# Kernel optimization log

Measured on AMD Instinct MI355X. Metric: run time of the kernel, lower is better.

## Reference

```python
import jax, jax.numpy as jnp
import numpy as np

V, E, D, B, L1, L2, C, NL = 32000, 300, 256, 64, 128, 128, 3, 10
BN_EPS = 1e-3  # tf.layers.batch_normalization default epsilon
BN_SCALE = 1.0 / np.sqrt(1.0 + BN_EPS)  # inference BN with moving mean=0, var=1


def setup_inputs() -> dict:
    key = jax.random.key(0)
    ks = iter(jax.random.split(key, 32))
    g = lambda shape, s=0.05: jax.random.normal(next(ks), shape, jnp.float32) * s
    inp = dict(
        embed_table=g((V, E), 1.0),
        W1_first=g((E, D)),            # layer 1 linear-BN-ReLU-1 (input dim = embed dim)
        W1_rest=g((NL - 1, D, D)),     # layers 2..10 linear-BN-ReLU-1
        b1=jnp.zeros((NL, D)),
        bn1_g=jnp.ones((NL, D)), bn1_b=jnp.zeros((NL, D)),
        W2=g((NL, 2 * D, D)),          # linear-BN-ReLU-2 on [x, aligned] concat
        b2=jnp.zeros((NL, D)),
        bn2_g=jnp.ones((NL, D)), bn2_b=jnp.zeros((NL, D)),
        Wg=g((NL, D, D)), bg=jnp.zeros((NL, D)),  # sigmoid gate
        Wf1=g((4 * D, 4 * D), 0.01), bf1=jnp.zeros((4 * D,)),
        Wf2=g((4 * D, 4 * D), 0.01), bf2=jnp.zeros((4 * D,)),
        Wout=g((4 * D, C)), bout=jnp.zeros((C,)),
        x1_ids=jax.random.randint(next(ks), (B, L1), 0, V, dtype=jnp.int32),
        x2_ids=jax.random.randint(next(ks), (B, L2), 0, V, dtype=jnp.int32),
    )
    return inp


def _lbr(x, W, b, g, be):
    # linear -> BN (inference: moving mean 0, var 1) -> ReLU
    y = jnp.dot(x, W) + b
    y = g * (y * BN_SCALE) + be
    return jax.nn.relu(y)


def _block(x1, x2):
    # pairwise squared euclidean distance: |a-b|^2 = |a|^2 + |b|^2 - 2 a.b
    sq1 = jnp.sum(x1 * x1, -1)                                  # [B,L1]
    sq2 = jnp.sum(x2 * x2, -1)                                  # [B,L2]
    edist = sq1[:, :, None] + sq2[:, None, :] \
        - 2.0 * jnp.einsum('bid,bjd->bij', x1, x2)              # [B,L1,L2]
    att = 1.0 / (1.0 + edist)
    # alpha = softmax(att^T) @ x1 ; beta = softmax(att) @ x2
    alpha = jnp.einsum('bji,bid->bjd',
                       jax.nn.softmax(jnp.swapaxes(att, 1, 2), axis=-1), x1)  # [B,L2,D]
    beta = jnp.einsum('bij,bjd->bid', jax.nn.softmax(att, axis=-1), x2)       # [B,L1,D]
    return alpha, beta


def reference(embed_table, W1_first, W1_rest, b1, bn1_g, bn1_b,
              W2, b2, bn2_g, bn2_b, Wg, bg,
              Wf1, bf1, Wf2, bf2, Wout, bout, x1_ids, x2_ids):
    x1 = embed_table[x1_ids]  # [B,L1,E]
    x2 = embed_table[x2_ids]  # [B,L2,E]
    for i in range(NL):
        W1 = W1_first if i == 0 else W1_rest[i - 1]
        h1 = _lbr(x1, W1, b1[i], bn1_g[i], bn1_b[i])
        h2 = _lbr(x2, W1, b1[i], bn1_g[i], bn1_b[i])
        alpha, beta = _block(h1, h2)
        v1 = _lbr(jnp.concatenate([h1, beta], -1), W2[i], b2[i], bn2_g[i], bn2_b[i])
        v2 = _lbr(jnp.concatenate([h2, alpha], -1), W2[i], b2[i], bn2_g[i], bn2_b[i])
        g1 = jax.nn.sigmoid(jnp.dot(h1, Wg[i]) + bg[i])
        g2 = jax.nn.sigmoid(jnp.dot(h2, Wg[i]) + bg[i])
        x1 = v1 * g1 + h1 * (1.0 - g1)
        x2 = v2 * g2 + h2 * (1.0 - g2)
    v = jnp.concatenate([x1.max(1), x2.max(1), x1.sum(1), x2.sum(1)], -1)  # [B,4D]
    t = jax.nn.relu(jnp.dot(v, Wf1) + bf1)   # op.linear default activation (ReLU); dropout off
    t = jax.nn.relu(jnp.dot(t, Wf2) + bf2)
    return jnp.dot(t, Wout) + bout           # logits [B,C]
```

## Files before the change

kernel.cpp:

```cpp
#include <hip/hip_runtime.h>
#include <hip/hip_bf16.h>
#include <cstddef>

#define NB 64
#define LL 128
#define EE 300
#define DD 256
#define NLAYERS 10
#define MROWS (NB * LL)

static constexpr float BN_SC = 0.9995003746877562f;

typedef unsigned short u16;
typedef __attribute__((ext_vector_type(4))) unsigned short us4;
typedef __attribute__((ext_vector_type(8))) unsigned short us8;
typedef __attribute__((ext_vector_type(8))) short bfrag;
typedef __attribute__((ext_vector_type(4))) float f4;

#define MFMA_B16(a, b, c) __builtin_amdgcn_mfma_f32_16x16x32_bf16(a, b, c, 0, 0, 0)

__device__ __forceinline__ u16 f2bf(float x) {
  union { float f; unsigned u; } v; v.f = x;
  unsigned r = v.u + 0x7FFFu + ((v.u >> 16) & 1u);
  return (u16)(r >> 16);
}
__device__ __forceinline__ float bf2f(u16 s) {
  union { unsigned u; float f; } v; v.u = (unsigned)s << 16;
  return v.f;
}
__device__ __forceinline__ float4 ld4(const float* p) { return *(const float4*)p; }

__device__ __forceinline__ void async16(void* lds, const void* g) {
  __builtin_amdgcn_global_load_lds(
      (const __attribute__((address_space(1))) unsigned int*)g,
      (__attribute__((address_space(3))) unsigned int*)lds, 16, 0, 0);
}

__device__ __forceinline__ void stage_tile(const u16* __restrict__ src, int ld,
                                           int r0, int k0, u16* lds, int t) {
  const int w = t >> 6;
  int c = w * 64 + (t & 63);
  async16((char*)lds + w * 1024,
          src + (size_t)(r0 + (c >> 2)) * ld + k0 + (c & 3) * 8);
  c += 256;
  async16((char*)lds + 4096 + w * 1024,
          src + (size_t)(r0 + (c >> 2)) * ld + k0 + (c & 3) * 8);
}

__device__ __forceinline__ void stage_tile64(const u16* __restrict__ src, int ld,
                                             int r0, int k0, u16* lds, int t) {
  const int w = t >> 6;
  const int c = t;
  async16((char*)lds + w * 1024,
          src + (size_t)(r0 + (c >> 2)) * ld + k0 + (c & 3) * 8);
}

__device__ __forceinline__ void mfma_step(const u16* As, const u16* Bs, int wm,
                                          int wn, int fr, int fq, f4 acc[4][4]) {
  bfrag a[4], b[4];
#pragma unroll
  for (int i = 0; i < 4; ++i)
    a[i] = *(const bfrag*)&As[(wm * 64 + i * 16 + fr) * 32 + fq * 8];
#pragma unroll
  for (int j = 0; j < 4; ++j)
    b[j] = *(const bfrag*)&Bs[(wn * 64 + j * 16 + fr) * 32 + fq * 8];
#pragma unroll
  for (int i = 0; i < 4; ++i)
#pragma unroll
    for (int j = 0; j < 4; ++j) acc[i][j] = MFMA_B16(a[i], b[j], acc[i][j]);
}

__device__ __forceinline__ void mfma_step_n64(const u16* As, const u16* Bs, int wm,
                                              int wn, int fr, int fq, f4 acc[4][2]) {
  bfrag a[4], b[2];
#pragma unroll
  for (int i = 0; i < 4; ++i)
    a[i] = *(const bfrag*)&As[(wm * 64 + i * 16 + fr) * 32 + fq * 8];
#pragma unroll
  for (int j = 0; j < 2; ++j)
    b[j] = *(const bfrag*)&Bs[(wn * 32 + j * 16 + fr) * 32 + fq * 8];
#pragma unroll
  for (int i = 0; i < 4; ++i)
#pragma unroll
    for (int j = 0; j < 2; ++j) acc[i][j] = MFMA_B16(a[i], b[j], acc[i][j]);
}

__device__ __forceinline__ void mfma_step2_n64(const u16* As, const u16* B2s,
                                               const u16* Bgs, int wm, int wn,
                                               int fr, int fq, f4 accv[4][2],
                                               f4 accg[4][2]) {
  bfrag a[4], b2[2], bg[2];
#pragma unroll
  for (int i = 0; i < 4; ++i)
    a[i] = *(const bfrag*)&As[(wm * 64 + i * 16 + fr) * 32 + fq * 8];
#pragma unroll
  for (int j = 0; j < 2; ++j) {
    b2[j] = *(const bfrag*)&B2s[(wn * 32 + j * 16 + fr) * 32 + fq * 8];
    bg[j] = *(const bfrag*)&Bgs[(wn * 32 + j * 16 + fr) * 32 + fq * 8];
  }
#pragma unroll
  for (int i = 0; i < 4; ++i)
#pragma unroll
    for (int j = 0; j < 2; ++j) {
      accv[i][j] = MFMA_B16(a[i], b2[j], accv[i][j]);
      accg[i][j] = MFMA_B16(a[i], bg[j], accg[i][j]);
    }
}

__device__ __forceinline__ bfrag gfrag(const u16* __restrict__ p, int ld, int row, int k) {
  return *(const bfrag*)(p + (size_t)row * ld + k);
}

__device__ __forceinline__ int eswz(int row, int colbyte) {
  return (row * 256 + colbyte) ^ ((row & 7) << 4);
}
__device__ __forceinline__ bfrag ldsE(const u16* E, int row, int colbyte) {
  return *(const bfrag*)((const char*)E + eswz(row, colbyte));
}

__device__ void txw_tile(const float* __restrict__ src, u16* __restrict__ dst,
                         int K, int N, int Kpad, int k0, int n0, int t,
                         float (*tileS)[65]) {
  __syncthreads();
  {
    const int kr = t >> 2, nc = (t & 3) * 16;
    const int k = k0 + kr;
#pragma unroll
    for (int j = 0; j < 16; j += 4) {
      float4 v = (k < K) ? ld4(src + (size_t)k * N + n0 + nc + j)
                         : make_float4(0.f, 0.f, 0.f, 0.f);
      tileS[kr][nc + j + 0] = v.x; tileS[kr][nc + j + 1] = v.y;
      tileS[kr][nc + j + 2] = v.z; tileS[kr][nc + j + 3] = v.w;
    }
  }
  __syncthreads();
  {
    const int nr = t >> 2, kc = (t & 3) * 16;
    us8 o0, o1;
#pragma unroll
    for (int j = 0; j < 8; ++j) {
      o0[j] = f2bf(tileS[kc + j][nr]);
      o1[j] = f2bf(tileS[kc + 8 + j][nr]);
    }
    u16* d = dst + (size_t)(n0 + nr) * Kpad + k0 + kc;
    *(us8*)d = o0;
    *(us8*)(d + 8) = o1;
  }
}

__global__ __launch_bounds__(256)
void k_prep(const float* __restrict__ W1f, const float* __restrict__ W1r,
            const float* __restrict__ W2, const float* __restrict__ Wg,
            const float* __restrict__ Wf1, const float* __restrict__ Wf2,
            u16* __restrict__ Wt1f, u16* __restrict__ Wt1r,
            u16* __restrict__ Wt2, u16* __restrict__ Wtg,
            u16* __restrict__ Wf1t, u16* __restrict__ Wf2t,
            const float* __restrict__ embed, const int* __restrict__ ids1,
            const int* __restrict__ ids2, u16* __restrict__ X1,
            u16* __restrict__ X2, u16* __restrict__ VPh, u16* __restrict__ VPl) {
  __shared__ float tileS[64][65];
  const int t = threadIdx.x;
  const int blk = blockIdx.x, nblk = gridDim.x;
  for (int it = blk; it < 20; it += nblk)
    txw_tile(W1f, Wt1f, 300, 256, 320, (it % 5) * 64, (it / 5) * 64, t, tileS);
  for (int it = blk; it < 144; it += nblk) {
    const int l = it / 16, r = it % 16;
    txw_tile(W1r + (size_t)l * 65536, Wt1r + (size_t)l * 65536, 256, 256, 256,
             (r % 4) * 64, (r / 4) * 64, t, tileS);
  }
  for (int it = blk; it < 320; it += nblk) {
    const int l = it / 32, r = it % 32;
    txw_tile(W2 + (size_t)l * 131072, Wt2 + (size_t)l * 131072, 512, 256, 512,
             (r % 8) * 64, (r / 8) * 64, t, tileS);
  }
  for (int it = blk; it < 160; it += nblk) {
    const int l = it / 16, r = it % 16;
    txw_tile(Wg + (size_t)l * 65536, Wtg + (size_t)l * 65536, 256, 256, 256,
             (r % 4) * 64, (r / 4) * 64, t, tileS);
  }
  for (int it = blk; it < 256; it += nblk)
    txw_tile(Wf1, Wf1t, 1024, 1024, 1024, (it % 16) * 64, (it / 16) * 64, t, tileS);
  for (int it = blk; it < 256; it += nblk)
    txw_tile(Wf2, Wf2t, 1024, 1024, 1024, (it % 16) * 64, (it / 16) * 64, t, tileS);
  for (int g = blk; g < 4096; g += nblk) {
    const int side = g & 1;
    const int* ids = side ? ids2 : ids1;
    u16* E = side ? X2 : X1;
    const int row = (g >> 1) * 4 + (t >> 6);
    const int lane = t & 63;
    const float* src = embed + (size_t)ids[row] * EE;
    u16* dst = E + (size_t)row * 320;
#pragma unroll
    for (int j = 0; j < 5; ++j) {
      const int c = lane + 64 * j;
      dst[c] = f2bf(c < EE ? src[c] : 0.f);
    }
  }
  for (int it = blk; it < 128; it += nblk) {
    const int arr = it & 1, row = 64 + (it >> 1);
    u16* dst = (arr ? VPl : VPh) + (size_t)row * 1024;
#pragma unroll
    for (int j = 0; j < 4; ++j) dst[t * 4 + j] = 0;
  }
}

__global__ __launch_bounds__(256, 2)
void mfma_lbr(const u16* __restrict__ A0, const u16* __restrict__ A1, int lda,
              int K, const u16* __restrict__ Wt, const float* __restrict__ bias,
              const float* __restrict__ gam, const float* __restrict__ bet,
              u16* __restrict__ O0, u16* __restrict__ O1,
              u16* __restrict__ HTa, u16* __restrict__ HTb,
              float* __restrict__ SQPa, float* __restrict__ SQPb) {
  const int side = blockIdx.z;
  const u16* A = side ? A1 : A0;
  u16* O = side ? O1 : O0;
  u16* HT = side ? HTb : HTa;
  float* SQP = side ? SQPb : SQPa;
  __shared__ u16 As[2][4096], Bs[2][2048];
  const int t = threadIdx.x;
  const int m0 = blockIdx.x * 128, n0 = blockIdx.y * 64;
  const int lane = t & 63, w = t >> 6, wm = w >> 1, wn = w & 1;
  const int fr = lane & 15, fq = lane >> 4;
  f4 acc[4][2] = {};
  const int nt = K / 32;
  stage_tile(A, lda, m0, 0, As[0], t);
  stage_tile64(Wt, K, n0, 0, Bs[0], t);
  __syncthreads();
  for (int ks = 0; ks < nt; ++ks) {
    const int cur = ks & 1;
    if (ks + 1 < nt) {
      stage_tile(A, lda, m0, (ks + 1) * 32, As[cur ^ 1], t);
      stage_tile64(Wt, K, n0, (ks + 1) * 32, Bs[cur ^ 1], t);
    }
    mfma_step_n64(As[cur], Bs[cur], wm, wn, fr, fq, acc);
    __syncthreads();
  }
  const int b = m0 >> 7;
  float rsq[4][4] = {};
#pragma unroll
  for (int nj = 0; nj < 2; ++nj) {
    const int n = n0 + wn * 32 + nj * 16 + fr;
    const float sc = gam[n] * BN_SC, bi = bias[n], be = bet[n];
#pragma unroll
    for (int mi = 0; mi < 4; ++mi) {
      const int m = m0 + wm * 64 + mi * 16 + fq * 4;
      us4 pk;
#pragma unroll
      for (int r = 0; r < 4; ++r) {
        const float x = sc * (acc[mi][nj][r] + bi) + be;
        const u16 hb = f2bf(fmaxf(x, 0.f));
        O[(size_t)(m + r) * DD + n] = hb;
        pk[r] = hb;
        const float h = bf2f(hb);
        rsq[mi][r] += h * h;
      }
      *(us4*)&HT[((size_t)b * DD + n) * LL + (m & 127)] = pk;
    }
  }
#pragma unroll
  for (int mi = 0; mi < 4; ++mi)
#pragma unroll
    for (int r = 0; r < 4; ++r) {
      float v = rsq[mi][r];
      v += __shfl_xor(v, 1, 64); v += __shfl_xor(v, 2, 64);
      v += __shfl_xor(v, 4, 64); v += __shfl_xor(v, 8, 64);
      rsq[mi][r] = v;
    }
  if (fr == 0) {
    const int p = blockIdx.y * 2 + wn;
#pragma unroll
    for (int mi = 0; mi < 4; ++mi)
#pragma unroll
      for (int r = 0; r < 4; ++r)
        SQP[(size_t)p * MROWS + m0 + wm * 64 + mi * 16 + fq * 4 + r] = rsq[mi][r];
  }
}

__global__ __launch_bounds__(256, 2)
void attf(const u16* __restrict__ H1, const u16* __restrict__ H2,
          const float* __restrict__ SQP1, const float* __restrict__ SQP2,
          const u16* __restrict__ HT1, const u16* __restrict__ HT2,
          u16* __restrict__ BETA, u16* __restrict__ ALPHA) {
  const int b = blockIdx.x, nh = blockIdx.y, side = blockIdx.z;
  __shared__ u16 Elds[128 * 128];
  __shared__ float sqs[2][128], rowp[2][128], colp[2][128];
  const int t = threadIdx.x, lane = t & 63, w = t >> 6;
  const int wm = w >> 1, wn = w & 1;
  const int fr = lane & 15, fq = lane >> 4;
  const int r0 = b * LL;
  if (t < 128) {
    float s = 0.f;
#pragma unroll
    for (int p = 0; p < 8; ++p) s += SQP1[(size_t)p * MROWS + r0 + t];
    sqs[0][t] = s;
  } else {
    const int u = t - 128;
    float s = 0.f;
#pragma unroll
    for (int p = 0; p < 8; ++p) s += SQP2[(size_t)p * MROWS + r0 + u];
    sqs[1][u] = s;
  }
  f4 acc[4][4] = {};
#pragma unroll
  for (int ks = 0; ks < 8; ++ks) {
    bfrag a[4], bv[4];
#pragma unroll
    for (int mi = 0; mi < 4; ++mi)
      a[mi] = gfrag(H1, DD, r0 + wm * 64 + mi * 16 + fr, ks * 32 + fq * 8);
#pragma unroll
    for (int nj = 0; nj < 4; ++nj)
      bv[nj] = gfrag(H2, DD, r0 + wn * 64 + nj * 16 + fr, ks * 32 + fq * 8);
#pragma unroll
    for (int mi = 0; mi < 4; ++mi)
#pragma unroll
      for (int nj = 0; nj < 4; ++nj) acc[mi][nj] = MFMA_B16(a[mi], bv[nj], acc[mi][nj]);
  }
  __syncthreads();
  float rp[4][4] = {}, cp[4] = {};
#pragma unroll
  for (int nj = 0; nj < 4; ++nj) {
    const int n = wn * 64 + nj * 16 + fr;
    const float s2 = sqs[1][n];
#pragma unroll
    for (int mi = 0; mi < 4; ++mi) {
      const int m = wm * 64 + mi * 16 + fq * 4;
#pragma unroll
      for (int r = 0; r < 4; ++r) {
        const float d = sqs[0][m + r] + s2 - 2.f * acc[mi][nj][r];
        const float e = __expf(1.f / (1.f + d));
        acc[mi][nj][r] = e;
        rp[mi][r] += e;
        cp[nj] += e;
      }
    }
  }
#pragma unroll
  for (int mi = 0; mi < 4; ++mi)
#pragma unroll
    for (int r = 0; r < 4; ++r) {
      float v = rp[mi][r];
      v += __shfl_xor(v, 1, 64); v += __shfl_xor(v, 2, 64);
      v += __shfl_xor(v, 4, 64); v += __shfl_xor(v, 8, 64);
      rp[mi][r] = v;
    }
#pragma unroll
  for (int nj = 0; nj < 4; ++nj) {
    float v = cp[nj];
    v += __shfl_xor(v, 16, 64); v += __shfl_xor(v, 32, 64);
    cp[nj] = v;
  }
  if (fr == 0)
#pragma unroll
    for (int mi = 0; mi < 4; ++mi)
#pragma unroll
      for (int r = 0; r < 4; ++r)
        rowp[wn][wm * 64 + mi * 16 + fq * 4 + r] = rp[mi][r];
  if (fq == 0)
#pragma unroll
    for (int nj = 0; nj < 4; ++nj)
      colp[wm][wn * 64 + nj * 16 + fr] = cp[nj];
  __syncthreads();
  if (side == 0) {
#pragma unroll
    for (int nj = 0; nj < 4; ++nj) {
      const int n = wn * 64 + nj * 16 + fr;
#pragma unroll
      for (int mi = 0; mi < 4; ++mi) {
        const int m = wm * 64 + mi * 16 + fq * 4;
#pragma unroll
        for (int r = 0; r < 4; ++r) {
          const float riv = 1.f / (rowp[0][m + r] + rowp[1][m + r]);
          *(u16*)((char*)Elds + eswz(m + r, n * 2)) = f2bf(acc[mi][nj][r] * riv);
        }
      }
    }
  } else {
#pragma unroll
    for (int nj = 0; nj < 4; ++nj) {
      const int n = wn * 64 + nj * 16 + fr;
      const float civ = 1.f / (colp[0][n] + colp[1][n]);
#pragma unroll
      for (int mi = 0; mi < 4; ++mi) {
        const int m = wm * 64 + mi * 16 + fq * 4;
        us4 pk;
#pragma unroll
        for (int r = 0; r < 4; ++r) pk[r] = f2bf(acc[mi][nj][r] * civ);
        *(us4*)((char*)Elds + eswz(n, m * 2)) = pk;
      }
    }
  }
  __syncthreads();
  const u16* HT = side ? HT1 : HT2;
  f4 pv[4][4] = {};
#pragma unroll
  for (int ks = 0; ks < 4; ++ks) {
    bfrag a[4], bv[4];
#pragma unroll
    for (int mi = 0; mi < 4; ++mi)
      a[mi] = ldsE(Elds, wm * 64 + mi * 16 + fr, ks * 64 + fq * 16);
#pragma unroll
    for (int nj = 0; nj < 4; ++nj)
      bv[nj] = gfrag(HT, LL, b * DD + nh * 128 + wn * 64 + nj * 16 + fr, ks * 32 + fq * 8);
#pragma unroll
    for (int mi = 0; mi < 4; ++mi)
#pragma unroll
      for (int nj = 0; nj < 4; ++nj) pv[mi][nj] = MFMA_B16(a[mi], bv[nj], pv[mi][nj]);
  }
  u16* O = side ? ALPHA : BETA;
#pragma unroll
  for (int nj = 0; nj < 4; ++nj) {
    const int n = nh * 128 + wn * 64 + nj * 16 + fr;
#pragma unroll
    for (int mi = 0; mi < 4; ++mi) {
      const int m = wm * 64 + mi * 16 + fq * 4;
#pragma unroll
      for (int r = 0; r < 4; ++r)
        O[(size_t)(r0 + m + r) * DD + n] = f2bf(pv[mi][nj][r]);
    }
  }
}

__global__ __launch_bounds__(256, 2)
void mfma_vg(const u16* __restrict__ Hbf1, const u16* __restrict__ Hbf2,
             const u16* __restrict__ BETA, const u16* __restrict__ ALPHA,
             const u16* __restrict__ Wt2, const u16* __restrict__ Wtg,
             const float* __restrict__ b2, const float* __restrict__ g2,
             const float* __restrict__ be2, const float* __restrict__ bgv,
             u16* __restrict__ X0, u16* __restrict__ X1p, int dopool,
             u16* __restrict__ VPh, u16* __restrict__ VPl) {
  const int side = blockIdx.z;
  const u16* H = side ? Hbf2 : Hbf1;
  const u16* CC = side ? ALPHA : BETA;
  u16* X = side ? X1p : X0;
  const int m0 = blockIdx.x * 128, n0 = blockIdx.y * 64;
  __shared__ u16 As[2][4096], B2s[2][2048], Bgs[2][2048];
  __shared__ float pmx[2][64], psm[2][64];
  const int t = threadIdx.x;
  const int lane = t & 63, w = t >> 6, wm = w >> 1, wn = w & 1;
  const int fr = lane & 15, fq = lane >> 4;
  f4 accv[4][2] = {}, accg[4][2] = {};
  stage_tile(H, DD, m0, 0, As[0], t);
  stage_tile64(Wt2, 2 * DD, n0, 0, B2s[0], t);
  stage_tile64(Wtg, DD, n0, 0, Bgs[0], t);
  __syncthreads();
  for (int ks = 0; ks < 16; ++ks) {
    const int cur = ks & 1;
    if (ks + 1 < 16) {
      const u16* Asrc = (ks + 1 < 8) ? H : CC;
      stage_tile(Asrc, DD, m0, ((ks + 1) & 7) * 32, As[cur ^ 1], t);
      stage_tile64(Wt2, 2 * DD, n0, (ks + 1) * 32, B2s[cur ^ 1], t);
      if (ks + 1 < 8) stage_tile64(Wtg, DD, n0, (ks + 1) * 32, Bgs[cur ^ 1], t);
    }
    if (ks < 8)
      mfma_step2_n64(As[cur], B2s[cur], Bgs[cur], wm, wn, fr, fq, accv, accg);
    else
      mfma_step_n64(As[cur], B2s[cur], wm, wn, fr, fq, accv);
    __syncthreads();
  }
  float pmax[2] = {-1e30f, -1e30f}, psum[2] = {0.f, 0.f};
#pragma unroll
  for (int nj = 0; nj < 2; ++nj) {
    const int n = n0 + wn * 32 + nj * 16 + fr;
    const float sc = g2[n] * BN_SC, bi = b2[n], be = be2[n], bgn = bgv[n];
#pragma unroll
    for (int mi = 0; mi < 4; ++mi) {
      const int m = m0 + wm * 64 + mi * 16 + fq * 4;
#pragma unroll
      for (int r = 0; r < 4; ++r) {
        const float v = fmaxf(sc * (accv[mi][nj][r] + bi) + be, 0.f);
        const float g = 1.f / (1.f + __expf(-(accg[mi][nj][r] + bgn)));
        const float h = bf2f(H[(size_t)(m + r) * DD + n]);
        const u16 xb = f2bf(v * g + h * (1.f - g));
        X[(size_t)(m + r) * DD + n] = xb;
        if (dopool) {
          const float xv = bf2f(xb);
          pmax[nj] = fmaxf(pmax[nj], xv);
          psum[nj] += xv;
        }
      }
    }
  }
  if (dopool) {
#pragma unroll
    for (int nj = 0; nj < 2; ++nj) {
      float mx = pmax[nj], sm = psum[nj];
      mx = fmaxf(mx, __shfl_xor(mx, 16, 64)); sm += __shfl_xor(sm, 16, 64);
      mx = fmaxf(mx, __shfl_xor(mx, 32, 64)); sm += __shfl_xor(sm, 32, 64);
      if (fq == 0) {
        pmx[wm][wn * 32 + nj * 16 + fr] = mx;
        psm[wm][wn * 32 + nj * 16 + fr] = sm;
      }
    }
    __syncthreads();
    if (t < 64) {
      const float mx = fmaxf(pmx[0][t], pmx[1][t]);
      const float sm = psm[0][t] + psm[1][t];
      const int b = m0 >> 7;
      const int col = n0 + t;
      const u16 mh = f2bf(mx);
      VPh[(size_t)b * 1024 + side * 256 + col] = mh;
      VPl[(size_t)b * 1024 + side * 256 + col] = f2bf(mx - bf2f(mh));
      const u16 sh = f2bf(sm);
      VPh[(size_t)b * 1024 + (2 + side) * 256 + col] = sh;
      VPl[(size_t)b * 1024 + (2 + side) * 256 + col] = f2bf(sm - bf2f(sh));
    }
  }
}

__global__ __launch_bounds__(256, 2)
void mlp_sk(const u16* __restrict__ Ah, const u16* __restrict__ Al,
            const u16* __restrict__ Wt, float* __restrict__ PART) {
  const int n0 = blockIdx.x * 128;
  const int k0 = blockIdx.y * 128;
  const int t = threadIdx.x, lane = t & 63, w = t >> 6;
  const int wm = w >> 1, wn = w & 1;
  const int fr = lane & 15, fq = lane >> 4;
  f4 acc[4][4] = {};
#pragma unroll
  for (int ks = 0; ks < 4; ++ks) {
    bfrag ah[4], al[4], bv[4];
#pragma unroll
    for (int mi = 0; mi < 4; ++mi) {
      ah[mi] = gfrag(Ah, 1024, wm * 64 + mi * 16 + fr, k0 + ks * 32 + fq * 8);
      al[mi] = gfrag(Al, 1024, wm * 64 + mi * 16 + fr, k0 + ks * 32 + fq * 8);
    }
#pragma unroll
    for (int nj = 0; nj < 4; ++nj)
      bv[nj] = gfrag(Wt, 1024, n0 + wn * 64 + nj * 16 + fr, k0 + ks * 32 + fq * 8);
#pragma unroll
    for (int mi = 0; mi < 4; ++mi)
#pragma unroll
      for (int nj = 0; nj < 4; ++nj) {
        acc[mi][nj] = MFMA_B16(ah[mi], bv[nj], acc[mi][nj]);
        acc[mi][nj] = MFMA_B16(al[mi], bv[nj], acc[mi][nj]);
      }
  }
#pragma unroll
  for (int nj = 0; nj < 4; ++nj) {
    const int n = n0 + wn * 64 + nj * 16 + fr;
#pragma unroll
    for (int mi = 0; mi < 4; ++mi) {
      const int m = wm * 64 + mi * 16 + fq * 4;
#pragma unroll
      for (int r = 0; r < 4; ++r)
        PART[((size_t)blockIdx.y * 128 + m + r) * 1024 + n] = acc[mi][nj][r];
    }
  }
}

__global__ __launch_bounds__(512)
void mlp_comb(const float* __restrict__ P, const float* __restrict__ bias,
              u16* __restrict__ Oh, u16* __restrict__ Ol,
              float* __restrict__ Of) {
#pragma unroll
  for (int e = 0; e < 8; ++e) {
    const int idx = blockIdx.x * 4096 + e * 512 + threadIdx.x;
    const int col = idx & 1023;
    float s = bias[col];
#pragma unroll
    for (int p = 0; p < 8; ++p) s += P[(size_t)p * 131072 + idx];
    s = fmaxf(s, 0.f);
    if (Oh) {
      const u16 h = f2bf(s);
      Oh[idx] = h;
      Ol[idx] = f2bf(s - bf2f(h));
    } else {
      Of[idx] = s;
    }
  }
}

__global__ __launch_bounds__(256)
void out_kernel(const float* __restrict__ T2, const float* __restrict__ Wout,
                const float* __restrict__ bout, float* __restrict__ out) {
  const int b = blockIdx.x;
  const int t = threadIdx.x;
  float a0 = 0.f, a1 = 0.f, a2 = 0.f;
  for (int k = t; k < 1024; k += 256) {
    const float x = T2[(size_t)b * 1024 + k];
    a0 = fmaf(x, Wout[k * 3 + 0], a0);
    a1 = fmaf(x, Wout[k * 3 + 1], a1);
    a2 = fmaf(x, Wout[k * 3 + 2], a2);
  }
  __shared__ float red[3][256];
  red[0][t] = a0; red[1][t] = a1; red[2][t] = a2;
  __syncthreads();
  for (int off = 128; off > 0; off >>= 1) {
    if (t < off) {
      red[0][t] += red[0][t + off];
      red[1][t] += red[1][t + off];
      red[2][t] += red[2][t + off];
    }
    __syncthreads();
  }
  if (t < 3) out[b * 3 + t] = red[t][0] + bout[t];
}

extern "C" void kernel_launch(void* const* d_in, const int* in_sizes, int n_in,
                              void* d_out, int out_size, void* d_ws, size_t ws_size,
                              hipStream_t stream) {
  (void)in_sizes; (void)n_in; (void)out_size; (void)ws_size;
  const float* embed = (const float*)d_in[0];
  const float* W1f   = (const float*)d_in[1];
  const float* W1r   = (const float*)d_in[2];
  const float* b1    = (const float*)d_in[3];
  const float* bn1g  = (const float*)d_in[4];
  const float* bn1b  = (const float*)d_in[5];
  const float* W2    = (const float*)d_in[6];
  const float* b2    = (const float*)d_in[7];
  const float* bn2g  = (const float*)d_in[8];
  const float* bn2b  = (const float*)d_in[9];
  const float* Wg    = (const float*)d_in[10];
  const float* bg    = (const float*)d_in[11];
  const float* Wf1   = (const float*)d_in[12];
  const float* bf1   = (const float*)d_in[13];
  const float* Wf2   = (const float*)d_in[14];
  const float* bf2   = (const float*)d_in[15];
  const float* Wout  = (const float*)d_in[16];
  const float* bout  = (const float*)d_in[17];
  const int* ids1    = (const int*)d_in[18];
  const int* ids2    = (const int*)d_in[19];

  char* wsp = (char*)d_ws;
  auto alloc = [&](size_t bytes) {
    char* p = wsp;
    wsp += (bytes + 255) & ~(size_t)255;
    return p;
  };
  u16* Hbf1  = (u16*)alloc((size_t)MROWS * DD * 2);
  u16* Hbf2  = (u16*)alloc((size_t)MROWS * DD * 2);
  u16* HT1   = (u16*)alloc((size_t)MROWS * DD * 2);
  u16* HT2   = (u16*)alloc((size_t)MROWS * DD * 2);
  u16* Xbf1  = (u16*)alloc((size_t)MROWS * 320 * 2);
  u16* Xbf2  = (u16*)alloc((size_t)MROWS * 320 * 2);
  u16* BETAb = (u16*)alloc((size_t)MROWS * DD * 2);
  u16* ALPHAb= (u16*)alloc((size_t)MROWS * DD * 2);
  float* SQP1= (float*)alloc((size_t)8 * MROWS * 4);
  float* SQP2= (float*)alloc((size_t)8 * MROWS * 4);
  u16* Wt1f  = (u16*)alloc((size_t)DD * 320 * 2);
  u16* Wt1r  = (u16*)alloc((size_t)9 * DD * DD * 2);
  u16* Wt2   = (u16*)alloc((size_t)10 * DD * 2 * DD * 2);
  u16* Wtg   = (u16*)alloc((size_t)10 * DD * DD * 2);
  u16* Wf1t  = (u16*)alloc((size_t)1024 * 1024 * 2);
  u16* Wf2t  = (u16*)alloc((size_t)1024 * 1024 * 2);
  u16* VPh   = (u16*)alloc((size_t)128 * 1024 * 2);
  u16* VPl   = (u16*)alloc((size_t)128 * 1024 * 2);
  u16* T1h   = (u16*)alloc((size_t)128 * 1024 * 2);
  u16* T1l   = (u16*)alloc((size_t)128 * 1024 * 2);
  float* T2f = (float*)alloc((size_t)128 * 1024 * 4);
  float* PART1 = (float*)alloc((size_t)8 * 128 * 1024 * 4);
  float* PART2 = (float*)alloc((size_t)8 * 128 * 1024 * 4);

  k_prep<<<512, 256, 0, stream>>>(W1f, W1r, W2, Wg, Wf1, Wf2,
                                  Wt1f, Wt1r, Wt2, Wtg, Wf1t, Wf2t,
                                  embed, ids1, ids2, Xbf1, Xbf2, VPh, VPl);

  for (int i = 0; i < NLAYERS; ++i) {
    const u16* Wt1 = (i == 0) ? Wt1f : (Wt1r + (size_t)(i - 1) * DD * DD);
    const int K1 = (i == 0) ? 320 : DD;
    mfma_lbr<<<dim3(MROWS / 128, 4, 2), 256, 0, stream>>>(
        Xbf1, Xbf2, K1, K1, Wt1, b1 + i * DD, bn1g + i * DD, bn1b + i * DD,
        Hbf1, Hbf2, HT1, HT2, SQP1, SQP2);
    attf<<<dim3(NB, 2, 2), 256, 0, stream>>>(Hbf1, Hbf2, SQP1, SQP2, HT1, HT2,
                                             BETAb, ALPHAb);
    mfma_vg<<<dim3(MROWS / 128, 4, 2), 256, 0, stream>>>(
        Hbf1, Hbf2, BETAb, ALPHAb, Wt2 + (size_t)i * DD * 2 * DD,
        Wtg + (size_t)i * DD * DD, b2 + i * DD, bn2g + i * DD, bn2b + i * DD,
        bg + i * DD, Xbf1, Xbf2, (i == NLAYERS - 1) ? 1 : 0, VPh, VPl);
  }
  mlp_sk<<<dim3(8, 8), 256, 0, stream>>>(VPh, VPl, Wf1t, PART1);
  mlp_comb<<<32, 512, 0, stream>>>(PART1, bf1, T1h, T1l, nullptr);
  mlp_sk<<<dim3(8, 8), 256, 0, stream>>>(T1h, T1l, Wf2t, PART2);
  mlp_comb<<<32, 512, 0, stream>>>(PART2, bf2, nullptr, nullptr, T2f);
  out_kernel<<<NB, 256, 0, stream>>>(T2f, Wout, bout, (float*)d_out);
}
```

Before: 524.3 us.

## Load MFMA fragments directly from global memory and fuse final MLP output

The LBR and value/gate GEMM kernels no longer double-buffer tiles through LDS with async loads and barriers. Each wave now reads its bf16 MFMA fragments straight from global memory in fully unrolled K loops, relying on L1/L2 caching for reuse between waves. Separately, the last MLP combine step is fused with the output projection: a new kernel reduces partials, applies ReLU and computes the 3 logits with wave shuffles, which removes the T2 buffer and one launch. The risk is that the global fragment loads are strided and less coalesced, and that data shared across waves is fetched repeatedly instead of once through LDS.

```diff
diff --git a/kernel.cpp b/kernel.cpp
--- a/kernel.cpp
+++ b/kernel.cpp
@@ -29,83 +29,6 @@
   return v.f;
 }
 __device__ __forceinline__ float4 ld4(const float* p) { return *(const float4*)p; }
-
-__device__ __forceinline__ void async16(void* lds, const void* g) {
-  __builtin_amdgcn_global_load_lds(
-      (const __attribute__((address_space(1))) unsigned int*)g,
-      (__attribute__((address_space(3))) unsigned int*)lds, 16, 0, 0);
-}
-
-__device__ __forceinline__ void stage_tile(const u16* __restrict__ src, int ld,
-                                           int r0, int k0, u16* lds, int t) {
-  const int w = t >> 6;
-  int c = w * 64 + (t & 63);
-  async16((char*)lds + w * 1024,
-          src + (size_t)(r0 + (c >> 2)) * ld + k0 + (c & 3) * 8);
-  c += 256;
-  async16((char*)lds + 4096 + w * 1024,
-          src + (size_t)(r0 + (c >> 2)) * ld + k0 + (c & 3) * 8);
-}
-
-__device__ __forceinline__ void stage_tile64(const u16* __restrict__ src, int ld,
-                                             int r0, int k0, u16* lds, int t) {
-  const int w = t >> 6;
-  const int c = t;
-  async16((char*)lds + w * 1024,
-          src + (size_t)(r0 + (c >> 2)) * ld + k0 + (c & 3) * 8);
-}
-
-__device__ __forceinline__ void mfma_step(const u16* As, const u16* Bs, int wm,
-                                          int wn, int fr, int fq, f4 acc[4][4]) {
-  bfrag a[4], b[4];
-#pragma unroll
-  for (int i = 0; i < 4; ++i)
-    a[i] = *(const bfrag*)&As[(wm * 64 + i * 16 + fr) * 32 + fq * 8];
-#pragma unroll
-  for (int j = 0; j < 4; ++j)
-    b[j] = *(const bfrag*)&Bs[(wn * 64 + j * 16 + fr) * 32 + fq * 8];
-#pragma unroll
-  for (int i = 0; i < 4; ++i)
-#pragma unroll
-    for (int j = 0; j < 4; ++j) acc[i][j] = MFMA_B16(a[i], b[j], acc[i][j]);
-}
-
-__device__ __forceinline__ void mfma_step_n64(const u16* As, const u16* Bs, int wm,
-                                              int wn, int fr, int fq, f4 acc[4][2]) {
-  bfrag a[4], b[2];
-#pragma unroll
-  for (int i = 0; i < 4; ++i)
-    a[i] = *(const bfrag*)&As[(wm * 64 + i * 16 + fr) * 32 + fq * 8];
-#pragma unroll
-  for (int j = 0; j < 2; ++j)
-    b[j] = *(const bfrag*)&Bs[(wn * 32 + j * 16 + fr) * 32 + fq * 8];
-#pragma unroll
-  for (int i = 0; i < 4; ++i)
-#pragma unroll
-    for (int j = 0; j < 2; ++j) acc[i][j] = MFMA_B16(a[i], b[j], acc[i][j]);
-}
-
-__device__ __forceinline__ void mfma_step2_n64(const u16* As, const u16* B2s,
-                                               const u16* Bgs, int wm, int wn,
-                                               int fr, int fq, f4 accv[4][2],
-                                               f4 accg[4][2]) {
-  bfrag a[4], b2[2], bg[2];
-#pragma unroll
-  for (int i = 0; i < 4; ++i)
-    a[i] = *(const bfrag*)&As[(wm * 64 + i * 16 + fr) * 32 + fq * 8];
-#pragma unroll
-  for (int j = 0; j < 2; ++j) {
-    b2[j] = *(const bfrag*)&B2s[(wn * 32 + j * 16 + fr) * 32 + fq * 8];
-    bg[j] = *(const bfrag*)&Bgs[(wn * 32 + j * 16 + fr) * 32 + fq * 8];
-  }
-#pragma unroll
-  for (int i = 0; i < 4; ++i)
-#pragma unroll
-    for (int j = 0; j < 2; ++j) {
-      accv[i][j] = MFMA_B16(a[i], b2[j], accv[i][j]);
-      accg[i][j] = MFMA_B16(a[i], bg[j], accg[i][j]);
-    }
-}
 
 __device__ __forceinline__ bfrag gfrag(const u16* __restrict__ p, int ld, int row, int k) {
   return *(const bfrag*)(p + (size_t)row * ld + k);
@@ -204,6 +127,26 @@
   }
 }
 
+template <int NT>
+__device__ __forceinline__ void lbr_core(const u16* __restrict__ Ap, int lda, int am0,
+                                         const u16* __restrict__ Bp, int ldb, int bn0,
+                                         int fr, int fq, f4 acc[4][2]) {
+#pragma unroll
+  for (int ks = 0; ks < NT; ++ks) {
+    bfrag a[4], b[2];
+#pragma unroll
+    for (int mi = 0; mi < 4; ++mi)
+      a[mi] = gfrag(Ap, lda, am0 + mi * 16 + fr, ks * 32 + fq * 8);
+#pragma unroll
+    for (int nj = 0; nj < 2; ++nj)
+      b[nj] = gfrag(Bp, ldb, bn0 + nj * 16 + fr, ks * 32 + fq * 8);
+#pragma unroll
+    for (int mi = 0; mi < 4; ++mi)
+#pragma unroll
+      for (int nj = 0; nj < 2; ++nj) acc[mi][nj] = MFMA_B16(a[mi], b[nj], acc[mi][nj]);
+  }
+}
+
 __global__ __launch_bounds__(256, 2)
 void mfma_lbr(const u16* __restrict__ A0, const u16* __restrict__ A1, int lda,
               int K, const u16* __restrict__ Wt, const float* __restrict__ bias,
@@ -216,25 +159,13 @@
   u16* O = side ? O1 : O0;
   u16* HT = side ? HTb : HTa;
   float* SQP = side ? SQPb : SQPa;
-  __shared__ u16 As[2][4096], Bs[2][2048];
   const int t = threadIdx.x;
   const int m0 = blockIdx.x * 128, n0 = blockIdx.y * 64;
   const int lane = t & 63, w = t >> 6, wm = w >> 1, wn = w & 1;
   const int fr = lane & 15, fq = lane >> 4;
   f4 acc[4][2] = {};
-  const int nt = K / 32;
-  stage_tile(A, lda, m0, 0, As[0], t);
-  stage_tile64(Wt, K, n0, 0, Bs[0], t);
-  __syncthreads();
-  for (int ks = 0; ks < nt; ++ks) {
-    const int cur = ks & 1;
-    if (ks + 1 < nt) {
-      stage_tile(A, lda, m0, (ks + 1) * 32, As[cur ^ 1], t);
-      stage_tile64(Wt, K, n0, (ks + 1) * 32, Bs[cur ^ 1], t);
-    }
-    mfma_step_n64(As[cur], Bs[cur], wm, wn, fr, fq, acc);
-    __syncthreads();
-  }
+  if (K == 256) lbr_core<8>(A, lda, m0 + wm * 64, Wt, K, n0 + wn * 32, fr, fq, acc);
+  else          lbr_core<10>(A, lda, m0 + wm * 64, Wt, K, n0 + wn * 32, fr, fq, acc);
   const int b = m0 >> 7;
   float rsq[4][4] = {};
 #pragma unroll
@@ -423,45 +354,59 @@
 __global__ __launch_bounds__(256, 2)
 void mfma_vg(const u16* __restrict__ Hbf1, const u16* __restrict__ Hbf2,
              const u16* __restrict__ BETA, const u16* __restrict__ ALPHA,
-             const u16* __restrict__ Wt2, const u16* __restrict__ Wtg,
-             const float* __restrict__ b2, const float* __restrict__ g2,
-             const float* __restrict__ be2, const float* __restrict__ bgv,
+             const u16* __restrict__ Wt2L, const u16* __restrict__ WtgL,
+             const float* __restrict__ b2v, const float* __restrict__ g2v,
+             const float* __restrict__ be2v, const float* __restrict__ bgv,
              u16* __restrict__ X0, u16* __restrict__ X1p, int dopool,
              u16* __restrict__ VPh, u16* __restrict__ VPl) {
   const int side = blockIdx.z;
   const u16* H = side ? Hbf2 : Hbf1;
   const u16* CC = side ? ALPHA : BETA;
   u16* X = side ? X1p : X0;
+  __shared__ float pmx[2][64], psm[2][64];
+  const int t = threadIdx.x, lane = t & 63, w = t >> 6;
+  const int wm = w >> 1, wn = w & 1;
+  const int fr = lane & 15, fq = lane >> 4;
   const int m0 = blockIdx.x * 128, n0 = blockIdx.y * 64;
-  __shared__ u16 As[2][4096], B2s[2][2048], Bgs[2][2048];
-  __shared__ float pmx[2][64], psm[2][64];
-  const int t = threadIdx.x;
-  const int lane = t & 63, w = t >> 6, wm = w >> 1, wn = w & 1;
-  const int fr = lane & 15, fq = lane >> 4;
   f4 accv[4][2] = {}, accg[4][2] = {};
-  stage_tile(H, DD, m0, 0, As[0], t);
-  stage_tile64(Wt2, 2 * DD, n0, 0, B2s[0], t);
-  stage_tile64(Wtg, DD, n0, 0, Bgs[0], t);
-  __syncthreads();
-  for (int ks = 0; ks < 16; ++ks) {
-    const int cur = ks & 1;
-    if (ks + 1 < 16) {
-      const u16* Asrc = (ks + 1 < 8) ? H : CC;
-      stage_tile(Asrc, DD, m0, ((ks + 1) & 7) * 32, As[cur ^ 1], t);
-      stage_tile64(Wt2, 2 * DD, n0, (ks + 1) * 32, B2s[cur ^ 1], t);
-      if (ks + 1 < 8) stage_tile64(Wtg, DD, n0, (ks + 1) * 32, Bgs[cur ^ 1], t);
-    }
-    if (ks < 8)
-      mfma_step2_n64(As[cur], B2s[cur], Bgs[cur], wm, wn, fr, fq, accv, accg);
-    else
-      mfma_step_n64(As[cur], B2s[cur], wm, wn, fr, fq, accv);
-    __syncthreads();
+#pragma unroll
+  for (int ks = 0; ks < 8; ++ks) {
+    bfrag a[4], b2f[2], bgf[2];
+#pragma unroll
+    for (int mi = 0; mi < 4; ++mi)
+      a[mi] = gfrag(H, DD, m0 + wm * 64 + mi * 16 + fr, ks * 32 + fq * 8);
+#pragma unroll
+    for (int nj = 0; nj < 2; ++nj) {
+      b2f[nj] = gfrag(Wt2L, 2 * DD, n0 + wn * 32 + nj * 16 + fr, ks * 32 + fq * 8);
+      bgf[nj] = gfrag(WtgL, DD, n0 + wn * 32 + nj * 16 + fr, ks * 32 + fq * 8);
+    }
+#pragma unroll
+    for (int mi = 0; mi < 4; ++mi)
+#pragma unroll
+      for (int nj = 0; nj < 2; ++nj) {
+        accv[mi][nj] = MFMA_B16(a[mi], b2f[nj], accv[mi][nj]);
+        accg[mi][nj] = MFMA_B16(a[mi], bgf[nj], accg[mi][nj]);
+      }
+  }
+#pragma unroll
+  for (int ks = 0; ks < 8; ++ks) {
+    bfrag a[4], b2f[2];
+#pragma unroll
+    for (int mi = 0; mi < 4; ++mi)
+      a[mi] = gfrag(CC, DD, m0 + wm * 64 + mi * 16 + fr, ks * 32 + fq * 8);
+#pragma unroll
+    for (int nj = 0; nj < 2; ++nj)
+      b2f[nj] = gfrag(Wt2L, 2 * DD, n0 + wn * 32 + nj * 16 + fr, DD + ks * 32 + fq * 8);
+#pragma unroll
+    for (int mi = 0; mi < 4; ++mi)
+#pragma unroll
+      for (int nj = 0; nj < 2; ++nj) accv[mi][nj] = MFMA_B16(a[mi], b2f[nj], accv[mi][nj]);
   }
   float pmax[2] = {-1e30f, -1e30f}, psum[2] = {0.f, 0.f};
 #pragma unroll
   for (int nj = 0; nj < 2; ++nj) {
     const int n = n0 + wn * 32 + nj * 16 + fr;
-    const float sc = g2[n] * BN_SC, bi = b2[n], be = be2[n], bgn = bgv[n];
+    const float sc = g2v[n] * BN_SC, bi = b2v[n], be = be2v[n], bgn = bgv[n];
 #pragma unroll
     for (int mi = 0; mi < 4; ++mi) {
       const int m = m0 + wm * 64 + mi * 16 + fq * 4;
@@ -550,8 +495,7 @@
 
 __global__ __launch_bounds__(512)
 void mlp_comb(const float* __restrict__ P, const float* __restrict__ bias,
-              u16* __restrict__ Oh, u16* __restrict__ Ol,
-              float* __restrict__ Of) {
+              u16* __restrict__ Oh, u16* __restrict__ Ol) {
 #pragma unroll
   for (int e = 0; e < 8; ++e) {
     const int idx = blockIdx.x * 4096 + e * 512 + threadIdx.x;
@@ -560,40 +504,50 @@
 #pragma unroll
     for (int p = 0; p < 8; ++p) s += P[(size_t)p * 131072 + idx];
     s = fmaxf(s, 0.f);
-    if (Oh) {
-      const u16 h = f2bf(s);
-      Oh[idx] = h;
-      Ol[idx] = f2bf(s - bf2f(h));
-    } else {
-      Of[idx] = s;
-    }
-  }
-}
-
-__global__ __launch_bounds__(256)
-void out_kernel(const float* __restrict__ T2, const float* __restrict__ Wout,
-                const float* __restrict__ bout, float* __restrict__ out) {
-  const int b = blockIdx.x;
+    const u16 h = f2bf(s);
+    Oh[idx] = h;
+    Ol[idx] = f2bf(s - bf2f(h));
+  }
+}
+
+__global__ __launch_bounds__(512)
+void mlp_comb_out(const float* __restrict__ P, const float* __restrict__ bias,
+                  const float* __restrict__ Wout, const float* __restrict__ bout,
+                  float* __restrict__ out) {
+  __shared__ float red[4][8][3];
   const int t = threadIdx.x;
-  float a0 = 0.f, a1 = 0.f, a2 = 0.f;
-  for (int k = t; k < 1024; k += 256) {
-    const float x = T2[(size_t)b * 1024 + k];
-    a0 = fmaf(x, Wout[k * 3 + 0], a0);
-    a1 = fmaf(x, Wout[k * 3 + 1], a1);
-    a2 = fmaf(x, Wout[k * 3 + 2], a2);
-  }
-  __shared__ float red[3][256];
-  red[0][t] = a0; red[1][t] = a1; red[2][t] = a2;
+  float a[4][3] = {};
+#pragma unroll
+  for (int e = 0; e < 8; ++e) {
+    const int idx = blockIdx.x * 4096 + e * 512 + t;
+    const int col = idx & 1023;
+    float s = bias[col];
+#pragma unroll
+    for (int p = 0; p < 8; ++p) s += P[(size_t)p * 131072 + idx];
+    s = fmaxf(s, 0.f);
+    const int lr = e >> 1;
+    a[lr][0] = fmaf(s, Wout[col * 3 + 0], a[lr][0]);
+    a[lr][1] = fmaf(s, Wout[col * 3 + 1], a[lr][1]);
+    a[lr][2] = fmaf(s, Wout[col * 3 + 2], a[lr][2]);
+  }
+  const int lane = t & 63, w = t >> 6;
+#pragma unroll
+  for (int lr = 0; lr < 4; ++lr)
+#pragma unroll
+    for (int c = 0; c < 3; ++c) {
+      float v = a[lr][c];
+#pragma unroll
+      for (int off = 32; off > 0; off >>= 1) v += __shfl_down(v, off, 64);
+      if (lane == 0) red[lr][w][c] = v;
+    }
   __syncthreads();
-  for (int off = 128; off > 0; off >>= 1) {
-    if (t < off) {
-      red[0][t] += red[0][t + off];
-      red[1][t] += red[1][t + off];
-      red[2][t] += red[2][t + off];
-    }
-    __syncthreads();
-  }
-  if (t < 3) out[b * 3 + t] = red[t][0] + bout[t];
+  if (t < 12) {
+    const int lr = t / 3, c = t % 3;
+    float s = bout[c];
+#pragma unroll
+    for (int w8 = 0; w8 < 8; ++w8) s += red[lr][w8][c];
+    out[(blockIdx.x * 4 + lr) * 3 + c] = s;
+  }
 }
 
 extern "C" void kernel_launch(void* const* d_in, const int* in_sizes, int n_in,
@@ -647,7 +601,6 @@
   u16* VPl   = (u16*)alloc((size_t)128 * 1024 * 2);
   u16* T1h   = (u16*)alloc((size_t)128 * 1024 * 2);
   u16* T1l   = (u16*)alloc((size_t)128 * 1024 * 2);
-  float* T2f = (float*)alloc((size_t)128 * 1024 * 4);
   float* PART1 = (float*)alloc((size_t)8 * 128 * 1024 * 4);
   float* PART2 = (float*)alloc((size_t)8 * 128 * 1024 * 4);
 
@@ -669,8 +622,7 @@
         bg + i * DD, Xbf1, Xbf2, (i == NLAYERS - 1) ? 1 : 0, VPh, VPl);
   }
   mlp_sk<<<dim3(8, 8), 256, 0, stream>>>(VPh, VPl, Wf1t, PART1);
-  mlp_comb<<<32, 512, 0, stream>>>(PART1, bf1, T1h, T1l, nullptr);
+  mlp_comb<<<32, 512, 0, stream>>>(PART1, bf1, T1h, T1l);
   mlp_sk<<<dim3(8, 8), 256, 0, stream>>>(T1h, T1l, Wf2t, PART2);
-  mlp_comb<<<32, 512, 0, stream>>>(PART2, bf2, nullptr, nullptr, T2f);
-  out_kernel<<<NB, 256, 0, stream>>>(T2f, Wout, bout, (float*)d_out);
-}
+  mlp_comb_out<<<16, 512, 0, stream>>>(PART2, bf2, Wout, bout, (float*)d_out);
+}
```

Result: slower. 733.5 us (+39.9%).
